# Kernel optimization log

Measured on AMD Instinct MI355X. Metric: run time of the kernel, lower is better.

Reference implementation:

```python
import jax, jax.numpy as jnp
import numpy as np
from math import sqrt

HEADS = 16
DIM_HEAD = 64
BETA = 1.0 / sqrt(DIM_HEAD)


def setup_inputs() -> dict:
    key = jax.random.key(0)
    k1, k2, k3 = jax.random.split(key, 3)
    b, n, dim = 2, 2048, 1024
    inner = HEADS * DIM_HEAD  # 1024
    x = jax.random.normal(k1, (b, n, dim), dtype=jnp.float32)
    W_qk = jax.random.normal(k2, (dim, 2 * inner), dtype=jnp.float32) * 0.02
    W_out = jax.random.normal(k3, (inner, dim), dtype=jnp.float32) * 0.02
    return {"x": x, "W_qk": W_qk, "W_out": W_out}


def reference(x, W_qk, W_out):
    # x: [b, n, dim]; to_qk: Linear(dim, 2*inner, bias=False)
    b, n, _ = x.shape
    qk = x @ W_qk                                   # [b, n, 2*inner]
    q, k = jnp.split(qk, 2, axis=-1)                # each [b, n, inner]
    # b n (h d) -> b h n d
    q = q.reshape(b, n, HEADS, DIM_HEAD).transpose(0, 2, 1, 3)
    k = k.reshape(b, n, HEADS, DIM_HEAD).transpose(0, 2, 1, 3)
    # beta-scaled scores
    scores = jnp.einsum('bhid,bhjd->bhij', q * BETA, k)  # [b, h, n, n]
    mask_value = -jnp.finfo(scores.dtype).max
    causal_mask = jnp.triu(jnp.ones((n, n), dtype=bool), k=1)
    scores = jnp.where(causal_mask, mask_value, scores)
    attn = jax.nn.softmax(scores, axis=-1)
    # K is reused as V
    out = jnp.einsum('bhij,bhjd->bhid', attn, k)    # [b, h, n, d]
    out = out.transpose(0, 2, 1, 3).reshape(b, n, HEADS * DIM_HEAD)
    # to_out Linear (dropout is identity in eval)
    return out @ W_out
```

## Files before the change

### kernel.cpp

```cpp
#include <hip/hip_runtime.h>
#include <hip/hip_bf16.h>
#include <math.h>

typedef short bf16x8 __attribute__((ext_vector_type(8)));
typedef float f32x4 __attribute__((ext_vector_type(4)));

__device__ __forceinline__ float bf2f(unsigned short u) {
    return __uint_as_float(((unsigned int)u) << 16);
}
__device__ __forceinline__ unsigned short f2bf(float f) {
    unsigned int u = __float_as_uint(f);
    u = (u + 0x7FFFu + ((u >> 16) & 1u)) >> 16;
    return (unsigned short)u;
}
__device__ __forceinline__ unsigned int pk2bf(float a, float b) {
    __hip_bfloat162 u = __float22bfloat162_rn(make_float2(a, b));
    return *(unsigned int*)&u;
}

#define ASYNC16(gp, lp)                                                        \
    __builtin_amdgcn_global_load_lds(                                          \
        (const __attribute__((address_space(1))) unsigned int*)(gp),           \
        (__attribute__((address_space(3))) unsigned int*)(lp), 16, 0, 0)

__global__ __launch_bounds__(256) void cast_x_kernel(const float* __restrict__ in,
                                                     unsigned short* __restrict__ out, int n) {
    int i = (blockIdx.x * 256 + threadIdx.x) * 8;
    if (i >= n) return;
    float4 a = *(const float4*)(in + i);
    float4 b = *(const float4*)(in + i + 4);
    bf16x8 v;
    v[0] = (short)f2bf(a.x); v[1] = (short)f2bf(a.y); v[2] = (short)f2bf(a.z); v[3] = (short)f2bf(a.w);
    v[4] = (short)f2bf(b.x); v[5] = (short)f2bf(b.y); v[6] = (short)f2bf(b.z); v[7] = (short)f2bf(b.w);
    *(bf16x8*)(out + i) = v;
}

__global__ __launch_bounds__(256) void transpose_cast_kernel(const float* __restrict__ in,
                                                             unsigned short* __restrict__ out,
                                                             int K, int N) {
    __shared__ float tile[32][33];
    int k0 = blockIdx.x * 32, n0 = blockIdx.y * 32;
    int tx = threadIdx.x & 31, ty = threadIdx.x >> 5;
    #pragma unroll
    for (int i = ty; i < 32; i += 8)
        tile[i][tx] = in[(size_t)(k0 + i) * N + (n0 + tx)];
    __syncthreads();
    #pragma unroll
    for (int i = ty; i < 32; i += 8)
        out[(size_t)(n0 + i) * K + (k0 + tx)] = f2bf(tile[tx][i]);
}

__global__ __launch_bounds__(256) void ktrans_kernel(const unsigned short* __restrict__ qkb,
                                                     unsigned short* __restrict__ kT) {
    __shared__ unsigned short tl[64][68];
    const int b = blockIdx.z;
    const int tok0 = blockIdx.x * 64;
    const int f0 = blockIdx.y * 64;
    const int r = threadIdx.x >> 4;
    const int c = (threadIdx.x & 15) * 4;
    #pragma unroll
    for (int i = 0; i < 4; ++i) {
        const int rr = r + 16 * i;
        ushort4 v = *(const ushort4*)(qkb + ((size_t)(b * 2048 + tok0 + rr)) * 2048 + 1024 + f0 + c);
        *(ushort4*)&tl[rr][c] = v;
    }
    __syncthreads();
    #pragma unroll
    for (int i = 0; i < 4; ++i) {
        const int fr = r + 16 * i;
        ushort4 v;
        v.x = tl[c + 0][fr]; v.y = tl[c + 1][fr]; v.z = tl[c + 2][fr]; v.w = tl[c + 3][fr];
        *(ushort4*)(kT + ((size_t)(b * 1024 + f0 + fr)) * 2048 + tok0 + c) = v;
    }
}

template <bool STORE_BF16>
__global__ __launch_bounds__(256) void gemm64k_kernel(const unsigned short* __restrict__ A,
                                                      const unsigned short* __restrict__ Bt,
                                                      void* __restrict__ C,
                                                      int K, int lda, int ldb, int ldc) {
    __shared__ unsigned short As[64 * 64];
    __shared__ unsigned short Bs[128 * 64];
    const int tid = threadIdx.x;
    const int wave = tid >> 6;
    const int lane = tid & 63;
    const int quad = lane >> 4;
    const int col  = lane & 15;
    const int sw   = col & 7;
    const int wm = (wave >> 1) * 32;
    const int wn = (wave & 1) * 64;
    const int m0 = blockIdx.x * 64, n0 = blockIdx.y * 128;

    f32x4 acc[2][4];
    #pragma unroll
    for (int i = 0; i < 2; ++i)
        #pragma unroll
        for (int j = 0; j < 4; ++j) { acc[i][j][0] = 0.f; acc[i][j][1] = 0.f; acc[i][j][2] = 0.f; acc[i][j][3] = 0.f; }

    const int r8 = lane >> 3;
    const int c8 = (lane & 7) ^ r8;

    for (int k0 = 0; k0 < K; k0 += 64) {
        __syncthreads();
        const unsigned short* ga = A  + (size_t)(m0 + wave * 8 + r8) * lda + k0 + c8 * 8;
        const unsigned short* gb = Bt + (size_t)(n0 + wave * 8 + r8) * ldb + k0 + c8 * 8;
        ASYNC16(ga,            &As[(wave * 8) * 64]);
        ASYNC16(ga + 32 * lda, &As[(32 + wave * 8) * 64]);
        ASYNC16(gb,            &Bs[(wave * 8) * 64]);
        ASYNC16(gb + 32 * ldb, &Bs[(32 + wave * 8) * 64]);
        ASYNC16(gb + 64 * ldb, &Bs[(64 + wave * 8) * 64]);
        ASYNC16(gb + 96 * ldb, &Bs[(96 + wave * 8) * 64]);
        __syncthreads();

        bf16x8 af[2][2], bf[4][2];
        #pragma unroll
        for (int mf = 0; mf < 2; ++mf) {
            const int base = (wm + mf * 16 + col) * 64;
            af[mf][0] = *(const bf16x8*)&As[base + ((quad    ) ^ sw) * 8];
            af[mf][1] = *(const bf16x8*)&As[base + ((quad + 4) ^ sw) * 8];
        }
        #pragma unroll
        for (int nf = 0; nf < 4; ++nf) {
            const int base = (wn + nf * 16 + col) * 64;
            bf[nf][0] = *(const bf16x8*)&Bs[base + ((quad    ) ^ sw) * 8];
            bf[nf][1] = *(const bf16x8*)&Bs[base + ((quad + 4) ^ sw) * 8];
        }
        #pragma unroll
        for (int mf = 0; mf < 2; ++mf)
            #pragma unroll
            for (int nf = 0; nf < 4; ++nf) {
                acc[mf][nf] = __builtin_amdgcn_mfma_f32_16x16x32_bf16(af[mf][0], bf[nf][0], acc[mf][nf], 0, 0, 0);
                acc[mf][nf] = __builtin_amdgcn_mfma_f32_16x16x32_bf16(af[mf][1], bf[nf][1], acc[mf][nf], 0, 0, 0);
            }
    }

    #pragma unroll
    for (int mf = 0; mf < 2; ++mf) {
        const int row0 = m0 + wm + mf * 16 + quad * 4;
        #pragma unroll
        for (int nf = 0; nf < 4; ++nf) {
            const int cc = n0 + wn + nf * 16 + col;
            #pragma unroll
            for (int r = 0; r < 4; ++r) {
                if (STORE_BF16)
                    ((unsigned short*)C)[(size_t)(row0 + r) * ldc + cc] = f2bf(acc[mf][nf][r]);
                else
                    ((float*)C)[(size_t)(row0 + r) * ldc + cc] = acc[mf][nf][r];
            }
        }
    }
}

__global__ __launch_bounds__(256, 4) void attn_v11_kernel(const unsigned short* __restrict__ qkb,
                                                          const unsigned short* __restrict__ kT,
                                                          unsigned short* __restrict__ aout) {
    __shared__ unsigned short Kbuf[2][2][64 * 64];
    __shared__ unsigned short Ps[4][16 * 64];

    const int bh = blockIdx.x;
    const int b = bh >> 4, h = bh & 15;
    const int qtile = 31 - (int)blockIdx.y;
    const int tid = threadIdx.x;
    const int wave = tid >> 6, lane = tid & 63, quad = lane >> 4, col = lane & 15;
    const int sw = col & 7;

    bf16x8 qa0, qa1;
    {
        const unsigned short* qp =
            qkb + ((size_t)(b * 2048 + qtile * 64 + wave * 16 + col)) * 2048 + h * 64;
        bf16x8 r0 = *(const bf16x8*)(qp + quad * 8);
        bf16x8 r1 = *(const bf16x8*)(qp + 32 + quad * 8);
        const float sc = 0.125f * 1.44269504088896f;
        #pragma unroll
        for (int i = 0; i < 8; ++i) {
            qa0[i] = (short)f2bf(bf2f((unsigned short)r0[i]) * sc);
            qa1[i] = (short)f2bf(bf2f((unsigned short)r1[i]) * sc);
        }
    }

    bf16x8 ones;
    #pragma unroll
    for (int i = 0; i < 8; ++i) ones[i] = (short)0x3F80;

    f32x4 accO[4];
    #pragma unroll
    for (int t = 0; t < 4; ++t) { accO[t][0] = 0.f; accO[t][1] = 0.f; accO[t][2] = 0.f; accO[t][3] = 0.f; }
    f32x4 accL = {0.f, 0.f, 0.f, 0.f};

    bf16x8 pa0p = {}, pa1p = {};
    bf16x8 vlo[4] = {}, vhi[4] = {};

    const int r8 = lane >> 3;
    const int c8 = (lane & 7) ^ r8;
    const unsigned short* knp =
        qkb + ((size_t)(b * 2048 + wave * 16 + r8)) * 2048 + 1024 + h * 64 + c8 * 8;
    const unsigned short* ktp = kT + ((size_t)(bh * 64 + wave * 16 + r8)) * 2048 + c8 * 8;

    auto issue = [&](int jt, int p) {
        const unsigned short* kn = knp + (size_t)jt * 64 * 2048;
        const unsigned short* kt = ktp + jt * 64;
        unsigned short* knl = &Kbuf[p][0][(wave * 16) * 64];
        unsigned short* ktl = &Kbuf[p][1][(wave * 16) * 64];
        ASYNC16(kn,            knl);
        ASYNC16(kn + 8 * 2048, knl + 8 * 64);
        ASYNC16(kt,            ktl);
        ASYNC16(kt + 8 * 2048, ktl + 8 * 64);
    };

    issue(0, 0);

    for (int jt = 0; jt <= qtile; ++jt) {
        const int cur = jt & 1;
        __builtin_amdgcn_s_barrier();
        if (jt < qtile) issue(jt + 1, cur ^ 1);
        if (jt < qtile) __builtin_amdgcn_s_waitcnt(0xF74);
        else            __builtin_amdgcn_s_waitcnt(0xF70);
        __builtin_amdgcn_s_barrier();
        __asm__ volatile("" ::: "memory");

        const unsigned short* Knc = &Kbuf[cur][0][0];
        const unsigned short* Ktc = &Kbuf[cur][1][0];

        const bool diag = (jt == qtile);
        const int tmax = diag ? wave : 3;

        f32x4 c[4];
        __builtin_amdgcn_s_setprio(1);
        #pragma unroll
        for (int t = 0; t < 4; ++t) {
            if (t <= tmax) {
                const int row = (t * 16 + col) * 64;
                bf16x8 ka0 = *(const bf16x8*)&Knc[row + (quad ^ sw) * 8];
                bf16x8 ka1 = *(const bf16x8*)&Knc[row + ((4 + quad) ^ sw) * 8];
                f32x4 ci = {-16.f, -16.f, -16.f, -16.f};
                ci = __builtin_amdgcn_mfma_f32_16x16x32_bf16(ka0, qa0, ci, 0, 0, 0);
                ci = __builtin_amdgcn_mfma_f32_16x16x32_bf16(ka1, qa1, ci, 0, 0, 0);
                c[t] = ci;
            }
        }
        if (jt) {
            #pragma unroll
            for (int t = 0; t < 4; ++t) {
                accO[t] = __builtin_amdgcn_mfma_f32_16x16x32_bf16(pa0p, vlo[t], accO[t], 0, 0, 0);
                accO[t] = __builtin_amdgcn_mfma_f32_16x16x32_bf16(pa1p, vhi[t], accO[t], 0, 0, 0);
            }
            accL = __builtin_amdgcn_mfma_f32_16x16x32_bf16(pa0p, ones, accL, 0, 0, 0);
            accL = __builtin_amdgcn_mfma_f32_16x16x32_bf16(pa1p, ones, accL, 0, 0, 0);
        }
        __builtin_amdgcn_s_setprio(0);

        unsigned int pw[4][2];
        #pragma unroll
        for (int t = 0; t < 4; ++t) {
            if (t <= tmax) {
                f32x4 ci = c[t];
                if (diag && t == wave) {
                    #pragma unroll
                    for (int r = 0; r < 4; ++r)
                        if (quad * 4 + r > col) ci[r] = -1e30f;
                }
                const float p0 = exp2f(ci[0]);
                const float p1 = exp2f(ci[1]);
                const float p2 = exp2f(ci[2]);
                const float p3 = exp2f(ci[3]);
                pw[t][0] = pk2bf(p0, p1);
                pw[t][1] = pk2bf(p2, p3);
            } else {
                pw[t][0] = 0u; pw[t][1] = 0u;
            }
        }

        unsigned short* psb = &Ps[wave][col * 64];
        #pragma unroll
        for (int t = 0; t < 4; ++t)
            *(uint2*)(psb + ((2 * t + (quad >> 1)) ^ sw) * 8 + (quad & 1) * 4) =
                make_uint2(pw[t][0], pw[t][1]);

        pa0p = *(const bf16x8*)(psb + (quad ^ sw) * 8);
        pa1p = *(const bf16x8*)(psb + ((4 + quad) ^ sw) * 8);

        #pragma unroll
        for (int t = 0; t < 4; ++t) {
            const int row = (t * 16 + col) * 64;
            vlo[t] = *(const bf16x8*)&Ktc[row + (quad ^ sw) * 8];
            vhi[t] = *(const bf16x8*)&Ktc[row + ((4 + quad) ^ sw) * 8];
        }
    }

    #pragma unroll
    for (int t = 0; t < 4; ++t) {
        accO[t] = __builtin_amdgcn_mfma_f32_16x16x32_bf16(pa0p, vlo[t], accO[t], 0, 0, 0);
        accO[t] = __builtin_amdgcn_mfma_f32_16x16x32_bf16(pa1p, vhi[t], accO[t], 0, 0, 0);
    }
    accL = __builtin_amdgcn_mfma_f32_16x16x32_bf16(pa0p, ones, accL, 0, 0, 0);
    accL = __builtin_amdgcn_mfma_f32_16x16x32_bf16(pa1p, ones, accL, 0, 0, 0);

    #pragma unroll
    for (int r = 0; r < 4; ++r) {
        const float inv = 1.f / accL[r];
        const size_t row = (size_t)b * 2048 + qtile * 64 + wave * 16 + quad * 4 + r;
        unsigned short* op = aout + row * 1024 + h * 64;
        op[col]      = f2bf(accO[0][r] * inv);
        op[16 + col] = f2bf(accO[1][r] * inv);
        op[32 + col] = f2bf(accO[2][r] * inv);
        op[48 + col] = f2bf(accO[3][r] * inv);
    }
}

extern "C" void kernel_launch(void* const* d_in, const int* in_sizes, int n_in,
                              void* d_out, int out_size, void* d_ws, size_t ws_size,
                              hipStream_t stream) {
    (void)in_sizes; (void)n_in; (void)out_size; (void)ws_size;
    const float* x    = (const float*)d_in[0];
    const float* Wqk  = (const float*)d_in[1];
    const float* Wout = (const float*)d_in[2];
    float* out = (float*)d_out;

    unsigned short* xb     = (unsigned short*)d_ws;
    unsigned short* Wqk_t  = xb     + (size_t)4096 * 1024;
    unsigned short* Wout_t = Wqk_t  + (size_t)2048 * 1024;
    unsigned short* qkb    = Wout_t + (size_t)1024 * 1024;
    unsigned short* aoutb  = qkb    + (size_t)4096 * 2048;
    unsigned short* kT     = xb;

    cast_x_kernel<<<dim3(4096 * 1024 / (256 * 8)), dim3(256), 0, stream>>>(x, xb, 4096 * 1024);
    transpose_cast_kernel<<<dim3(32, 64), dim3(256), 0, stream>>>(Wqk, Wqk_t, 1024, 2048);
    transpose_cast_kernel<<<dim3(32, 32), dim3(256), 0, stream>>>(Wout, Wout_t, 1024, 1024);

    gemm64k_kernel<true><<<dim3(64, 16), dim3(256), 0, stream>>>(
        xb, Wqk_t, (void*)qkb, 1024, 1024, 1024, 2048);

    ktrans_kernel<<<dim3(32, 16, 2), dim3(256), 0, stream>>>(qkb, kT);

    attn_v11_kernel<<<dim3(32, 32), dim3(256), 0, stream>>>(qkb, kT, aoutb);

    gemm64k_kernel<false><<<dim3(64, 8), dim3(256), 0, stream>>>(
        aoutb, Wout_t, (void*)out, 1024, 1024, 1024, 1024);
}
```

Before: 175.2 us.

## Double-buffer LDS tiles in GEMM kernel to overlap loads with MFMA

Converts the bf16 MFMA GEMM to a two-stage LDS pipeline. The next K-tile is issued with async global-to-LDS loads while the current tile is computed, and partial vmcnt waits plus raw barriers replace the full syncthreads pair. It also raises wave priority around the MFMA block. This doubles LDS use per block, which may lower occupancy, and relies on hand-coded waitcnt encodings being correct.

```diff
diff --git a/kernel.cpp b/kernel.cpp
--- a/kernel.cpp
+++ b/kernel.cpp
@@ -75,12 +75,12 @@
 }
 
 template <bool STORE_BF16>
-__global__ __launch_bounds__(256) void gemm64k_kernel(const unsigned short* __restrict__ A,
+__global__ __launch_bounds__(256) void gemm_db_kernel(const unsigned short* __restrict__ A,
                                                       const unsigned short* __restrict__ Bt,
                                                       void* __restrict__ C,
                                                       int K, int lda, int ldb, int ldc) {
-    __shared__ unsigned short As[64 * 64];
-    __shared__ unsigned short Bs[128 * 64];
+    __shared__ unsigned short As[2][64 * 64];
+    __shared__ unsigned short Bs[2][128 * 64];
     const int tid = threadIdx.x;
     const int wave = tid >> 6;
     const int lane = tid & 63;
@@ -99,32 +99,52 @@
 
     const int r8 = lane >> 3;
     const int c8 = (lane & 7) ^ r8;
-
-    for (int k0 = 0; k0 < K; k0 += 64) {
-        __syncthreads();
-        const unsigned short* ga = A  + (size_t)(m0 + wave * 8 + r8) * lda + k0 + c8 * 8;
-        const unsigned short* gb = Bt + (size_t)(n0 + wave * 8 + r8) * ldb + k0 + c8 * 8;
-        ASYNC16(ga,            &As[(wave * 8) * 64]);
-        ASYNC16(ga + 32 * lda, &As[(32 + wave * 8) * 64]);
-        ASYNC16(gb,            &Bs[(wave * 8) * 64]);
-        ASYNC16(gb + 32 * ldb, &Bs[(32 + wave * 8) * 64]);
-        ASYNC16(gb + 64 * ldb, &Bs[(64 + wave * 8) * 64]);
-        ASYNC16(gb + 96 * ldb, &Bs[(96 + wave * 8) * 64]);
-        __syncthreads();
+    const unsigned short* gab = A  + (size_t)(m0 + wave * 8 + r8) * lda + c8 * 8;
+    const unsigned short* gbb = Bt + (size_t)(n0 + wave * 8 + r8) * ldb + c8 * 8;
+
+    auto issue = [&](int k0, int p) {
+        const unsigned short* ga = gab + k0;
+        const unsigned short* gb = gbb + k0;
+        ASYNC16(ga,            &As[p][(wave * 8) * 64]);
+        ASYNC16(ga + 32 * lda, &As[p][(32 + wave * 8) * 64]);
+        ASYNC16(gb,            &Bs[p][(wave * 8) * 64]);
+        ASYNC16(gb + 32 * ldb, &Bs[p][(32 + wave * 8) * 64]);
+        ASYNC16(gb + 64 * ldb, &Bs[p][(64 + wave * 8) * 64]);
+        ASYNC16(gb + 96 * ldb, &Bs[p][(96 + wave * 8) * 64]);
+    };
+
+    issue(0, 0);
+
+    const int nk = K >> 6;
+    for (int kt = 0; kt < nk; ++kt) {
+        const int cur = kt & 1;
+        __builtin_amdgcn_s_barrier();
+        if (kt + 1 < nk) {
+            issue((kt + 1) << 6, cur ^ 1);
+            __builtin_amdgcn_s_waitcnt(0xF76);
+        } else {
+            __builtin_amdgcn_s_waitcnt(0xF70);
+        }
+        __builtin_amdgcn_s_barrier();
+        __asm__ volatile("" ::: "memory");
+
+        const unsigned short* Asc = &As[cur][0];
+        const unsigned short* Bsc = &Bs[cur][0];
 
         bf16x8 af[2][2], bf[4][2];
         #pragma unroll
         for (int mf = 0; mf < 2; ++mf) {
             const int base = (wm + mf * 16 + col) * 64;
-            af[mf][0] = *(const bf16x8*)&As[base + ((quad    ) ^ sw) * 8];
-            af[mf][1] = *(const bf16x8*)&As[base + ((quad + 4) ^ sw) * 8];
+            af[mf][0] = *(const bf16x8*)&Asc[base + ((quad    ) ^ sw) * 8];
+            af[mf][1] = *(const bf16x8*)&Asc[base + ((quad + 4) ^ sw) * 8];
         }
         #pragma unroll
         for (int nf = 0; nf < 4; ++nf) {
             const int base = (wn + nf * 16 + col) * 64;
-            bf[nf][0] = *(const bf16x8*)&Bs[base + ((quad    ) ^ sw) * 8];
-            bf[nf][1] = *(const bf16x8*)&Bs[base + ((quad + 4) ^ sw) * 8];
-        }
+            bf[nf][0] = *(const bf16x8*)&Bsc[base + ((quad    ) ^ sw) * 8];
+            bf[nf][1] = *(const bf16x8*)&Bsc[base + ((quad + 4) ^ sw) * 8];
+        }
+        __builtin_amdgcn_s_setprio(1);
         #pragma unroll
         for (int mf = 0; mf < 2; ++mf)
             #pragma unroll
@@ -132,6 +152,7 @@
                 acc[mf][nf] = __builtin_amdgcn_mfma_f32_16x16x32_bf16(af[mf][0], bf[nf][0], acc[mf][nf], 0, 0, 0);
                 acc[mf][nf] = __builtin_amdgcn_mfma_f32_16x16x32_bf16(af[mf][1], bf[nf][1], acc[mf][nf], 0, 0, 0);
             }
+        __builtin_amdgcn_s_setprio(0);
     }
 
     #pragma unroll
@@ -327,13 +348,13 @@
     transpose_cast_kernel<<<dim3(32, 64), dim3(256), 0, stream>>>(Wqk, Wqk_t, 1024, 2048);
     transpose_cast_kernel<<<dim3(32, 32), dim3(256), 0, stream>>>(Wout, Wout_t, 1024, 1024);
 
-    gemm64k_kernel<true><<<dim3(64, 16), dim3(256), 0, stream>>>(
+    gemm_db_kernel<true><<<dim3(64, 16), dim3(256), 0, stream>>>(
         xb, Wqk_t, (void*)qkb, 1024, 1024, 1024, 2048);
 
     ktrans_kernel<<<dim3(32, 16, 2), dim3(256), 0, stream>>>(qkb, kT);
 
     attn_v11_kernel<<<dim3(32, 32), dim3(256), 0, stream>>>(qkb, kT, aoutb);
 
-    gemm64k_kernel<false><<<dim3(64, 8), dim3(256), 0, stream>>>(
+    gemm_db_kernel<false><<<dim3(64, 8), dim3(256), 0, stream>>>(
         aoutb, Wout_t, (void*)out, 1024, 1024, 1024, 1024);
 }
```

After: 176.4 us. Within noise of the previous version (+0.7%).
